# Optimization experiments

Measured on AMD Instinct MI355X. Metric: run time of the kernel, lower is better.

Reference implementation:

```python
import jax, jax.numpy as jnp
import numpy as np

A = 8        # n_agents
NACT = 16    # n_actions
R = 64       # rnn_hidden_dim
OBS = 128    # obs_shape
ATTN = 64    # attn_dim
HID = 256    # hidden_dim
INP = 152    # input_shape = obs + n_actions + n_agents
E = 2048     # episode_num
TW = 1.0     # teammate_loss_weight
WW = 1.0     # world_loss_weight


def _lin(key, out_d, in_d):
    k1, k2 = jax.random.split(key)
    s = 1.0 / np.sqrt(in_d)
    w = jax.random.uniform(k1, (out_d, in_d), minval=-s, maxval=s, dtype=jnp.float32)
    b = jax.random.uniform(k2, (out_d,), minval=-s, maxval=s, dtype=jnp.float32)
    return w, b


def setup_inputs() -> dict:
    key = jax.random.key(0)
    ks = jax.random.split(key, 16)
    rows = E * A
    d = {}
    d['inputs'] = jax.random.normal(ks[0], (rows, INP), dtype=jnp.float32)
    d['hidden_state'] = jax.random.normal(ks[1], (rows, R), dtype=jnp.float32)
    d['obs'] = jax.random.normal(ks[2], (rows, OBS), dtype=jnp.float32)
    d['obs_next'] = jax.random.normal(ks[3], (rows, OBS), dtype=jnp.float32)
    d['u'] = jax.random.randint(ks[4], (rows, 1), 0, NACT, dtype=jnp.int64 if jax.config.jax_enable_x64 else jnp.int32)
    d['fc1_w'], d['fc1_b'] = _lin(ks[5], R, INP)
    d['gru_w_ih'], d['gru_b_ih'] = _lin(ks[6], 3 * R, R)
    d['gru_w_hh'], d['gru_b_hh'] = _lin(ks[7], 3 * R, R)
    d['tm_w1'], d['tm_b1'] = _lin(ks[8], HID, R + A)
    d['tm_w2'], d['tm_b2'] = _lin(ks[9], NACT, HID)
    d['wm_w1'], d['wm_b1'] = _lin(ks[10], HID, OBS + A * NACT)
    d['wm_w2'], d['wm_b2'] = _lin(ks[11], OBS, HID)
    d['wq_w'], d['wq_b'] = _lin(ks[12], ATTN, 2 * OBS)
    d['wk_w'], d['wk_b'] = _lin(ks[13], ATTN, NACT)
    d['wv1_w'], d['wv1_b'] = _lin(ks[14], ATTN, R + NACT)
    d['wv2_w'], d['wv2_b'] = _lin(ks[15], NACT, ATTN)
    return d


def reference(inputs, hidden_state, obs, obs_next, u,
              fc1_w, fc1_b, gru_w_ih, gru_b_ih, gru_w_hh, gru_b_hh,
              tm_w1, tm_b1, tm_w2, tm_b2,
              wm_w1, wm_b1, wm_w2, wm_b2,
              wq_w, wq_b, wk_w, wk_b, wv1_w, wv1_b, wv2_w, wv2_b):
    sg = jax.lax.stop_gradient
    rows = inputs.shape[0]
    Ep = rows // A  # episode_num

    # --- GRU agent trunk ---
    x = jax.nn.relu(inputs @ fc1_w.T + fc1_b)
    h_in = hidden_state.reshape(-1, R)
    gi = x @ gru_w_ih.T + gru_b_ih
    gh = h_in @ gru_w_hh.T + gru_b_hh
    i_r, i_z, i_n = jnp.split(gi, 3, axis=-1)
    h_r, h_z, h_n = jnp.split(gh, 3, axis=-1)
    r = jax.nn.sigmoid(i_r + h_r)
    z = jax.nn.sigmoid(i_z + h_z)
    n = jnp.tanh(i_n + r * h_n)
    h = (1.0 - z) * n + z * h_in  # (rows, R)

    eyeA = jnp.eye(A, dtype=h.dtype)
    off = 1.0 - eyeA  # (A,A) zero on diagonal

    # --- teammate model: h_repeat[e,i,j] = h[e,j] with diagonal zeroed ---
    hd = sg(h).reshape(Ep, A, R)
    hr = jnp.broadcast_to(hd[:, None, :, :], (Ep, A, A, R)) * off[None, :, :, None]
    dj = jnp.broadcast_to(eyeA[None, None], (Ep, A, A, A)) * off[None, :, :, None]
    inp_t = jnp.concatenate([hr.reshape(-1, R), dj.reshape(-1, A)], axis=-1)
    actions = jax.nn.relu(inp_t @ tm_w1.T + tm_b1) @ tm_w2.T + tm_b2  # (Ep*A*A, NACT)

    # --- teammate CE loss (masked mean over all Ep*A*A rows) ---
    labels = jnp.broadcast_to(u.reshape(Ep, 1, A), (Ep, A, A)).reshape(-1)
    mask = jnp.broadcast_to(off[None], (Ep, A, A)).reshape(-1)
    logp = jax.nn.log_softmax(actions, axis=-1)
    ce = -jnp.take_along_axis(logp, labels[:, None], axis=1)[:, 0]
    loss1 = (ce * mask).mean() * TW

    # --- mask own action, world model ---
    am = (actions.reshape(Ep, A, A, NACT) * off[None, :, :, None]).reshape(rows, A, NACT)
    am_det = sg(am)
    w_in = jnp.concatenate([obs, am_det.reshape(rows, A * NACT)], axis=-1)
    o_next_hat = jax.nn.relu(w_in @ wm_w1.T + wm_b1) @ wm_w2.T + wm_b2  # (rows, OBS)
    loss2 = jnp.mean((o_next_hat - obs_next) ** 2) * WW

    # --- reflection: masked attention aggregation over teammates ---
    query = jnp.concatenate([obs, sg(o_next_hat)], axis=-1) @ wq_w.T + wq_b  # (rows, ATTN)
    key = (am_det.reshape(-1, NACT) @ wk_w.T + wk_b).reshape(rows, A, ATTN)
    hrep = jnp.broadcast_to(h.reshape(Ep, 1, A, R), (Ep, A, A, R)).reshape(-1, R)
    inps_v = jnp.concatenate([hrep, am_det.reshape(-1, NACT)], axis=-1)
    value = (jax.nn.relu(inps_v @ wv1_w.T + wv1_b) @ wv2_w.T + wv2_b).reshape(rows, A, NACT)
    scores = jnp.einsum('bd,bjd->bj', query / jnp.sqrt(jnp.float32(ATTN)), key).reshape(Ep, A, A)
    scores = jnp.where(eyeA[None].astype(bool), jnp.float32(-1e9), scores)  # self-exclusion
    attn = jax.nn.softmax(scores, axis=-1).reshape(rows, A, 1)
    q_reflect = jnp.sum(value * attn, axis=1)  # (rows, NACT)

    return q_reflect, h, loss1, loss2
```

## Files before the change

### kernel.cpp

```cpp
#include <hip/hip_runtime.h>
#include <math.h>

#define E_NUM 2048
#define A_N   8
#define ROWS  (E_NUM*A_N)

typedef __attribute__((ext_vector_type(8))) short bf16x8;
typedef __attribute__((ext_vector_type(4))) float f32x4;

__device__ __forceinline__ unsigned short f2bf(float x) {
  unsigned int u = __float_as_uint(x);
  return (unsigned short)((u + 0x7FFFu + ((u >> 16) & 1u)) >> 16);
}
__device__ __forceinline__ ushort4 f2bf4(float4 v) {
  return make_ushort4(f2bf(v.x), f2bf(v.y), f2bf(v.z), f2bf(v.w));
}
#define MFMA16(a,b,c) __builtin_amdgcn_mfma_f32_16x16x32_bf16(a,b,c,0,0,0)

#define T_WK   0
#define T_WV1  1024
#define T_WV2  6144
#define TMB    7168
#define B_WM1  9216
#define B_WM2  41984
#define B_WQ   58368
#define B_TM1  66560
#define B_TM2  74752
#define B_FC1  76800
#define B_WIH  81920
#define B_WHH  88064
#define O_ACT  94208
#define O_QRY  356352
#define O_L1P  1404928
#define O_L2P  1405440

#define DO_H   262144
#define DO_L1  1310720
#define DO_L2  1310721

#define LD4(p) (*(const float4*)(p))

struct PrepP {
  const float* tsrc[3]; int tO[3], tK[3], tOff[3];
  const float* ssrc[8]; int sO[8], sK[8], sKs[8], sSt[8], sOff[8];
  const float* tm_w1; const float* tm_b1;
};

__global__ __launch_bounds__(256) void k_prep(PrepP p, float* __restrict__ ws,
                                              unsigned short* __restrict__ wsu) {
  int bid = blockIdx.x;
  if (bid < 24) {
    int b = bid >> 3, sl = bid & 7;
    const float* s = p.tsrc[b];
    float* d = ws + p.tOff[b];
    int O = p.tO[b], K = p.tK[b], n = O * K;
    for (int i = sl * 256 + threadIdx.x; i < n; i += 2048) {
      int o = i / K, k = i - o * K;
      d[k * O + o] = s[i];
    }
  } else if (bid < 152) {
    int q = bid - 24, m = q >> 4, sub = q & 15;
    const float* src = p.ssrc[m];
    unsigned short* dst = wsu + p.sOff[m];
    int K = p.sK[m], Ks = p.sKs[m], stride = p.sSt[m], n = p.sO[m] * K, S = K >> 5;
    for (int f = sub * 256 + threadIdx.x; f < n; f += 16 * 256) {
      int j = f & 7, l = (f >> 3) & 63, rest = f >> 9;
      int s = rest % S, c = rest / S;
      int row = c * 16 + (l & 15), col = s * 32 + ((l >> 4) << 3) + j;
      dst[f] = (col < Ks) ? f2bf(src[row * stride + col]) : (unsigned short)0;
    }
  } else {
    int i = (bid - 152) * 256 + threadIdx.x;
    int j = i >> 8, o = i & 255;
    ws[TMB + i] = p.tm_b1[o] + p.tm_w1[o * 72 + 64 + j];
  }
}

__global__ __launch_bounds__(512) void k_trunk(
    const float* __restrict__ inp, const float* __restrict__ hin,
    const unsigned short* __restrict__ fc1bf, const unsigned short* __restrict__ wihbf,
    const unsigned short* __restrict__ whhbf,
    const float* __restrict__ fc1_b, const float* __restrict__ bih, const float* __restrict__ bhh,
    float* __restrict__ hout)
{
  __shared__ __align__(16) unsigned short in_b[32 * 168];
  __shared__ __align__(16) unsigned short x_b[32 * 72];
  __shared__ __align__(16) unsigned short h_b[32 * 72];
  int tid = threadIdx.x, w = tid >> 6, lane = tid & 63;
  int lo = lane & 15, hi = lane >> 4;
  int row0 = blockIdx.x * 32;
  int c = w & 3, rt = w >> 2;

  for (int i = tid; i < 1216; i += 512) {
    int e = i << 2;
    int r = e / 152, cc = e - r * 152;
    float4 v = LD4(inp + (size_t)(row0 + r) * 152 + cc);
    *(ushort4*)(in_b + r * 168 + cc) = f2bf4(v);
  }
  if (tid < 256) { int r = tid >> 3, cc = tid & 7; in_b[r * 168 + 152 + cc] = 0; }
  {
    int r = tid >> 4, cc = (tid & 15) << 2;
    float4 v = LD4(hin + (size_t)(row0 + r) * 64 + cc);
    *(ushort4*)(h_b + r * 72 + cc) = f2bf4(v);
  }
  __syncthreads();

  bf16x8 wf1[5];
#pragma unroll
  for (int s = 0; s < 5; s++)
    wf1[s] = *(const bf16x8*)(fc1bf + (size_t)((c * 5 + s) * 64 + lane) * 8);
  f32x4 acc = {0, 0, 0, 0};
#pragma unroll
  for (int s = 0; s < 5; s++) {
    bf16x8 af = *(const bf16x8*)(in_b + (rt * 16 + lo) * 168 + s * 32 + hi * 8);
    acc = MFMA16(af, wf1[s], acc);
  }
  float fb = fc1_b[16 * c + lo];
#pragma unroll
  for (int r = 0; r < 4; r++)
    x_b[(rt * 16 + hi * 4 + r) * 72 + 16 * c + lo] = f2bf(fmaxf(acc[r] + fb, 0.f));
  __syncthreads();

  bf16x8 wfi[3][2], wfh[3][2];
#pragma unroll
  for (int t = 0; t < 3; t++)
#pragma unroll
    for (int s = 0; s < 2; s++) {
      int chunk = c + 4 * t;
      wfi[t][s] = *(const bf16x8*)(wihbf + (size_t)((chunk * 2 + s) * 64 + lane) * 8);
      wfh[t][s] = *(const bf16x8*)(whhbf + (size_t)((chunk * 2 + s) * 64 + lane) * 8);
    }
  f32x4 ai[3], ah[3];
#pragma unroll
  for (int t = 0; t < 3; t++) { ai[t] = {0,0,0,0}; ah[t] = {0,0,0,0}; }
#pragma unroll
  for (int s = 0; s < 2; s++) {
    bf16x8 ax  = *(const bf16x8*)(x_b + (rt * 16 + lo) * 72 + s * 32 + hi * 8);
    bf16x8 ahv = *(const bf16x8*)(h_b + (rt * 16 + lo) * 72 + s * 32 + hi * 8);
#pragma unroll
    for (int t = 0; t < 3; t++) {
      ai[t] = MFMA16(ax,  wfi[t][s], ai[t]);
      ah[t] = MFMA16(ahv, wfh[t][s], ah[t]);
    }
  }
  int col = 16 * c + lo;
  float b_ir = bih[col],       b_hr = bhh[col];
  float b_iz = bih[64 + col],  b_hz = bhh[64 + col];
  float b_in = bih[128 + col], b_hn = bhh[128 + col];
#pragma unroll
  for (int r = 0; r < 4; r++) {
    size_t grow = (size_t)(row0 + rt * 16 + hi * 4 + r);
    float rg = 1.f / (1.f + expf(-(ai[0][r] + b_ir + ah[0][r] + b_hr)));
    float zg = 1.f / (1.f + expf(-(ai[1][r] + b_iz + ah[1][r] + b_hz)));
    float ng = tanhf(fmaf(rg, ah[2][r] + b_hn, ai[2][r] + b_in));
    float h0 = hin[grow * 64 + col];
    hout[grow * 64 + col] = (1.f - zg) * ng + zg * h0;
  }
}

__global__ __launch_bounds__(512) void k_tm(
    const float* __restrict__ h,
    const unsigned short* __restrict__ w1b, const unsigned short* __restrict__ w2b,
    const float* __restrict__ tmB, const float* __restrict__ b2,
    const int* __restrict__ u,
    float* __restrict__ act, float* __restrict__ l1p)
{
  __shared__ __align__(16) unsigned short in_s[32 * 72];
  __shared__ __align__(16) unsigned short hid_s[32 * 264];
  __shared__ float red[512];
  int tid = threadIdx.x, w = tid >> 6, lane = tid & 63;
  int lo = lane & 15, hi = lane >> 4;
  int row0 = blockIdx.x * 32;
  {
    int r = tid >> 4, cc = (tid & 15) << 2;
    float4 v = LD4(h + (size_t)(row0 + r) * 64 + cc);
    *(ushort4*)(in_s + r * 72 + cc) = f2bf4(v);
  }
  bf16x8 wf1[2][2];
#pragma unroll
  for (int cc = 0; cc < 2; cc++)
#pragma unroll
    for (int s = 0; s < 2; s++)
      wf1[cc][s] = *(const bf16x8*)(w1b + (size_t)(((2 * w + cc) * 2 + s) * 64 + lane) * 8);
  __syncthreads();
  f32x4 acc[2][2];
#pragma unroll
  for (int rt = 0; rt < 2; rt++) { acc[rt][0] = {0,0,0,0}; acc[rt][1] = {0,0,0,0}; }
#pragma unroll
  for (int s = 0; s < 2; s++)
#pragma unroll
    for (int rt = 0; rt < 2; rt++) {
      bf16x8 af = *(const bf16x8*)(in_s + (rt * 16 + lo) * 72 + s * 32 + hi * 8);
      acc[rt][0] = MFMA16(af, wf1[0][s], acc[rt][0]);
      acc[rt][1] = MFMA16(af, wf1[1][s], acc[rt][1]);
    }
#pragma unroll
  for (int rt = 0; rt < 2; rt++)
#pragma unroll
    for (int r = 0; r < 4; r++) {
      int rowl = rt * 16 + hi * 4 + r, j = (hi * 4 + r) & 7;
      float v0 = acc[rt][0][r] + tmB[j * 256 + 32 * w + lo];
      float v1 = acc[rt][1][r] + tmB[j * 256 + 32 * w + 16 + lo];
      hid_s[rowl * 264 + 32 * w + lo]      = f2bf(fmaxf(v0, 0.f));
      hid_s[rowl * 264 + 32 * w + 16 + lo] = f2bf(fmaxf(v1, 0.f));
    }
  __syncthreads();
  float ces = 0.f;
  if (w < 2) {
    bf16x8 wf2[8];
#pragma unroll
    for (int s = 0; s < 8; s++)
      wf2[s] = *(const bf16x8*)(w2b + (size_t)(s * 64 + lane) * 8);
    f32x4 a2 = {0, 0, 0, 0};
#pragma unroll
    for (int s = 0; s < 8; s++) {
      bf16x8 af = *(const bf16x8*)(hid_s + (w * 16 + lo) * 264 + s * 32 + hi * 8);
      a2 = MFMA16(af, wf2[s], a2);
    }
    float b2c = b2[lo];
#pragma unroll
    for (int r = 0; r < 4; r++) {
      int rowl = w * 16 + hi * 4 + r;
      float v = a2[r] + b2c;
      act[(size_t)(row0 + rowl) * 16 + lo] = v;
      float m = v;
      m = fmaxf(m, __shfl_xor(m, 1));
      m = fmaxf(m, __shfl_xor(m, 2));
      m = fmaxf(m, __shfl_xor(m, 4));
      m = fmaxf(m, __shfl_xor(m, 8));
      float se = expf(v - m);
      se += __shfl_xor(se, 1);
      se += __shfl_xor(se, 2);
      se += __shfl_xor(se, 4);
      se += __shfl_xor(se, 8);
      int lbl = u[row0 + rowl];
      float vl = __shfl(v, (lane & 48) + lbl);
      if (lo == 0) ces += -(vl - m - logf(se));
    }
  }
  red[tid] = ces;
  __syncthreads();
  for (int st = 256; st > 0; st >>= 1) {
    if (tid < st) red[tid] += red[tid + st];
    __syncthreads();
  }
  if (tid == 0) l1p[blockIdx.x] = red[0];
}

__global__ __launch_bounds__(512) void k_wm(
    const float* __restrict__ obs, const float* __restrict__ act,
    const unsigned short* __restrict__ w1b, const unsigned short* __restrict__ w2b,
    const unsigned short* __restrict__ wqb,
    const float* __restrict__ b1, const float* __restrict__ b2, const float* __restrict__ bq,
    const float* __restrict__ obsn,
    float* __restrict__ qry, float* __restrict__ l2p)
{
  __shared__ __align__(16) unsigned short in_s[32 * 264];
  __shared__ __align__(16) unsigned short q_in[32 * 264];
  __shared__ __align__(16) unsigned short act_bs[4 * 128];
  __shared__ float red[512];
  int tid = threadIdx.x, w = tid >> 6, lane = tid & 63;
  int lo = lane & 15, hi = lane >> 4;
  int row0 = blockIdx.x * 32, e0 = row0 >> 3;
  if (tid < 128) {
    float4 v = LD4(act + (size_t)e0 * 128 + (tid << 2));
    *(ushort4*)(act_bs + (tid << 2)) = f2bf4(v);
  }
  for (int i = tid; i < 1024; i += 512) {
    int r = i >> 5, c = (i & 31) << 2;
    float4 v = LD4(obs + (size_t)(row0 + r) * 128 + c);
    ushort4 u4 = f2bf4(v);
    *(ushort4*)(in_s + r * 264 + c) = u4;
    *(ushort4*)(q_in + r * 264 + c) = u4;
  }
  bf16x8 wf1[2][8], wf2[8];
#pragma unroll
  for (int cc = 0; cc < 2; cc++)
#pragma unroll
    for (int s = 0; s < 8; s++)
      wf1[cc][s] = *(const bf16x8*)(w1b + (size_t)(((2 * w + cc) * 8 + s) * 64 + lane) * 8);
#pragma unroll
  for (int s = 0; s < 8; s++)
    wf2[s] = *(const bf16x8*)(w2b + (size_t)((w * 8 + s) * 64 + lane) * 8);
  __syncthreads();
  for (int i = tid; i < 1024; i += 512) {
    int r = i >> 5, c = (i & 31) << 2;
    int j = c >> 4, ii = r & 7;
    ushort4 v = (j == ii) ? make_ushort4(0, 0, 0, 0)
                          : *(const ushort4*)(act_bs + (r >> 3) * 128 + c);
    *(ushort4*)(in_s + r * 264 + 128 + c) = v;
  }
  __syncthreads();
  f32x4 acc[2][2];
#pragma unroll
  for (int rt = 0; rt < 2; rt++) { acc[rt][0] = {0,0,0,0}; acc[rt][1] = {0,0,0,0}; }
#pragma unroll
  for (int s = 0; s < 8; s++)
#pragma unroll
    for (int rt = 0; rt < 2; rt++) {
      bf16x8 af = *(const bf16x8*)(in_s + (rt * 16 + lo) * 264 + s * 32 + hi * 8);
      acc[rt][0] = MFMA16(af, wf1[0][s], acc[rt][0]);
      acc[rt][1] = MFMA16(af, wf1[1][s], acc[rt][1]);
    }
  float b1a = b1[32 * w + lo], b1b = b1[32 * w + 16 + lo];
  __syncthreads();
#pragma unroll
  for (int rt = 0; rt < 2; rt++)
#pragma unroll
    for (int r = 0; r < 4; r++) {
      int rowl = rt * 16 + hi * 4 + r;
      in_s[rowl * 264 + 32 * w + lo]      = f2bf(fmaxf(acc[rt][0][r] + b1a, 0.f));
      in_s[rowl * 264 + 32 * w + 16 + lo] = f2bf(fmaxf(acc[rt][1][r] + b1b, 0.f));
    }
  __syncthreads();
  f32x4 acc2[2];
  acc2[0] = {0, 0, 0, 0}; acc2[1] = {0, 0, 0, 0};
#pragma unroll
  for (int s = 0; s < 8; s++)
#pragma unroll
    for (int rt = 0; rt < 2; rt++) {
      bf16x8 af = *(const bf16x8*)(in_s + (rt * 16 + lo) * 264 + s * 32 + hi * 8);
      acc2[rt] = MFMA16(af, wf2[s], acc2[rt]);
    }
  int col = 16 * w + lo;
  float b2c = b2[col];
  float ms = 0.f;
#pragma unroll
  for (int rt = 0; rt < 2; rt++)
#pragma unroll
    for (int r = 0; r < 4; r++) {
      int rowl = rt * 16 + hi * 4 + r;
      float v = acc2[rt][r] + b2c;
      q_in[rowl * 264 + 128 + col] = f2bf(v);
      float d = v - obsn[(size_t)(row0 + rowl) * 128 + col];
      ms = fmaf(d, d, ms);
    }
  __syncthreads();
  {
    int c = w & 3, rt = w >> 2;
    bf16x8 wf3[8];
#pragma unroll
    for (int s = 0; s < 8; s++)
      wf3[s] = *(const bf16x8*)(wqb + (size_t)((c * 8 + s) * 64 + lane) * 8);
    f32x4 aq = {0, 0, 0, 0};
#pragma unroll
    for (int s = 0; s < 8; s++) {
      bf16x8 af = *(const bf16x8*)(q_in + (rt * 16 + lo) * 264 + s * 32 + hi * 8);
      aq = MFMA16(af, wf3[s], aq);
    }
    float bqc = bq[16 * c + lo];
#pragma unroll
    for (int r = 0; r < 4; r++) {
      int row = row0 + rt * 16 + hi * 4 + r;
      qry[(size_t)row * 64 + 16 * c + lo] = aq[r] + bqc;
    }
  }
  red[tid] = ms;
  __syncthreads();
  for (int st = 256; st > 0; st >>= 1) {
    if (tid < st) red[tid] += red[tid + st];
    __syncthreads();
  }
  if (tid == 0) l2p[blockIdx.x] = red[0];
}

__global__ __launch_bounds__(256) void k_kva(
    const float* __restrict__ h, const float* __restrict__ act,
    const float* __restrict__ ws, const float* __restrict__ bk,
    const float* __restrict__ bv1, const float* __restrict__ bv2,
    const float* __restrict__ qry, const float* __restrict__ l1p,
    const float* __restrict__ l2p, float* __restrict__ qout)
{
  __shared__ __align__(16) float in_s[32 * 80];
  __shared__ __align__(16) float hid_s[32 * 64];
  __shared__ __align__(16) float key_s[32 * 68];
  __shared__ float val_s[32 * 16];
  __shared__ float qs[4][64];
  __shared__ float red2[256];
  int tid = threadIdx.x, w = tid >> 6, lane = tid & 63;
  int row0 = blockIdx.x * 32;
  if (blockIdx.x == 0) {
    float s1 = l1p[tid] + l1p[tid + 256];
    float s2 = l2p[tid] + l2p[tid + 256];
    red2[tid] = s1;
    __syncthreads();
    for (int s = 128; s > 0; s >>= 1) {
      if (tid < s) red2[tid] += red2[tid + s];
      __syncthreads();
    }
    float S1 = red2[0];
    __syncthreads();
    red2[tid] = s2;
    __syncthreads();
    for (int s = 128; s > 0; s >>= 1) {
      if (tid < s) red2[tid] += red2[tid + s];
      __syncthreads();
    }
    if (tid == 0) {
      qout[DO_L1] = S1 * 7.f / 131072.f;
      qout[DO_L2] = red2[0] / 2097152.f;
    }
    __syncthreads();
  }
  for (int i = tid; i < 512; i += 256) {
    int r = i >> 4, c = (i & 15) << 2;
    *(float4*)(in_s + r * 80 + c) = LD4(h + (size_t)(row0 + r) * 64 + c);
  }
  if (tid < 128) {
    int r = tid >> 2, c = (tid & 3) << 2;
    *(float4*)(in_s + r * 80 + 64 + c) = LD4(act + (size_t)(row0 + r) * 16 + c);
  }
  float qreg[8];
#pragma unroll
  for (int rr = 0; rr < 8; rr++)
    qreg[rr] = qry[(size_t)(row0 + w * 8 + rr) * 64 + lane];
  __syncthreads();
  const float* w1T = ws + T_WV1;
  const float* w2T = ws + T_WV2;
  const float* wkT = ws + T_WK;
  float acc[8];
#pragma unroll
  for (int r = 0; r < 8; r++) acc[r] = bv1[lane];
  for (int k = 0; k < 80; k += 4) {
    float b[4];
#pragma unroll
    for (int j = 0; j < 4; j++) b[j] = w1T[(k + j) * 64 + lane];
#pragma unroll
    for (int r = 0; r < 8; r++) {
      float4 a = LD4(in_s + (w * 8 + r) * 80 + k);
      acc[r] = fmaf(a.x, b[0], fmaf(a.y, b[1], fmaf(a.z, b[2], fmaf(a.w, b[3], acc[r]))));
    }
  }
#pragma unroll
  for (int r = 0; r < 8; r++) hid_s[(w * 8 + r) * 64 + lane] = fmaxf(acc[r], 0.f);
  float ka[8];
#pragma unroll
  for (int r = 0; r < 8; r++) ka[r] = bk[lane];
  for (int k = 0; k < 16; k += 4) {
    float b[4];
#pragma unroll
    for (int j = 0; j < 4; j++) b[j] = wkT[(k + j) * 64 + lane];
#pragma unroll
    for (int r = 0; r < 8; r++) {
      float4 a = LD4(in_s + (w * 8 + r) * 80 + 64 + k);
      ka[r] = fmaf(a.x, b[0], fmaf(a.y, b[1], fmaf(a.z, b[2], fmaf(a.w, b[3], ka[r]))));
    }
  }
#pragma unroll
  for (int r = 0; r < 8; r++) key_s[(w * 8 + r) * 68 + lane] = ka[r];
  int col = lane & 15, kq = lane >> 4;
  float a2[8] = {0, 0, 0, 0, 0, 0, 0, 0};
  for (int kk = 0; kk < 16; kk += 4) {
    int k = kq * 16 + kk;
    float b[4];
#pragma unroll
    for (int j = 0; j < 4; j++) b[j] = w2T[(k + j) * 16 + col];
#pragma unroll
    for (int r = 0; r < 8; r++) {
      float4 a = LD4(hid_s + (w * 8 + r) * 64 + k);
      a2[r] = fmaf(a.x, b[0], fmaf(a.y, b[1], fmaf(a.z, b[2], fmaf(a.w, b[3], a2[r]))));
    }
  }
#pragma unroll
  for (int r = 0; r < 8; r++) {
    a2[r] += __shfl_xor(a2[r], 16);
    a2[r] += __shfl_xor(a2[r], 32);
  }
  if (lane < 16) {
#pragma unroll
    for (int r = 0; r < 8; r++) val_s[(w * 8 + r) * 16 + col] = a2[r] + bv2[col];
  }
  int j = lane >> 3, p = lane & 7;
  for (int rr = 0; rr < 8; rr++) {
    int b = row0 + w * 8 + rr;
    qs[w][lane] = qreg[rr];
    const float* krow = key_s + (w * 8 + j) * 68;
    float s = 0.f;
#pragma unroll
    for (int t = 0; t < 8; t++) {
      int d = p * 8 + t;
      s = fmaf(qs[w][d], krow[d], s);
    }
    s += __shfl_xor(s, 1);
    s += __shfl_xor(s, 2);
    s += __shfl_xor(s, 4);
    float score = (j == rr) ? -1e9f : s * 0.125f;
    float sc[8];
    float m = -1e30f;
#pragma unroll
    for (int jj = 0; jj < 8; jj++) {
      sc[jj] = __shfl(score, jj * 8);
      m = fmaxf(m, sc[jj]);
    }
    float ssum = 0.f;
#pragma unroll
    for (int jj = 0; jj < 8; jj++) { sc[jj] = expf(sc[jj] - m); ssum += sc[jj]; }
    float inv = 1.f / ssum;
    int c = lane & 15, g = lane >> 4;
    const float* vb = val_s + w * 8 * 16;
    float outv = sc[g] * inv * vb[g * 16 + c] + sc[g + 4] * inv * vb[(g + 4) * 16 + c];
    outv += __shfl_xor(outv, 16);
    outv += __shfl_xor(outv, 32);
    if (lane < 16) qout[(size_t)b * 16 + lane] = outv;
  }
}

extern "C" void kernel_launch(void* const* d_in, const int* in_sizes, int n_in,
                              void* d_out, int out_size, void* d_ws, size_t ws_size,
                              hipStream_t stream) {
  const float* inputs   = (const float*)d_in[0];
  const float* hidden   = (const float*)d_in[1];
  const float* obs      = (const float*)d_in[2];
  const float* obs_next = (const float*)d_in[3];
  const int*   u        = (const int*)d_in[4];
  const float* fc1_w = (const float*)d_in[5];   const float* fc1_b = (const float*)d_in[6];
  const float* wih   = (const float*)d_in[7];   const float* bih   = (const float*)d_in[8];
  const float* whh   = (const float*)d_in[9];   const float* bhh   = (const float*)d_in[10];
  const float* tm_w1 = (const float*)d_in[11];  const float* tm_b1 = (const float*)d_in[12];
  const float* tm_w2 = (const float*)d_in[13];  const float* tm_b2 = (const float*)d_in[14];
  const float* wm_w1 = (const float*)d_in[15];  const float* wm_b1 = (const float*)d_in[16];
  const float* wm_w2 = (const float*)d_in[17];  const float* wm_b2 = (const float*)d_in[18];
  const float* wq_w  = (const float*)d_in[19];  const float* wq_b  = (const float*)d_in[20];
  const float* wk_w  = (const float*)d_in[21];  const float* wk_b  = (const float*)d_in[22];
  const float* wv1_w = (const float*)d_in[23];  const float* wv1_b = (const float*)d_in[24];
  const float* wv2_w = (const float*)d_in[25];  const float* wv2_b = (const float*)d_in[26];

  float* ws   = (float*)d_ws;
  unsigned short* wsu = (unsigned short*)d_ws;
  float* out  = (float*)d_out;
  float* hbuf = out + DO_H;

  PrepP p;
  const float* tsr[3] = {wk_w, wv1_w, wv2_w};
  int tO[3]  = {64, 64, 16};
  int tK[3]  = {16, 80, 64};
  int tOf[3] = {T_WK, T_WV1, T_WV2};
  for (int i = 0; i < 3; i++) { p.tsrc[i] = tsr[i]; p.tO[i] = tO[i]; p.tK[i] = tK[i]; p.tOff[i] = tOf[i]; }
  const float* ssr[8] = {wm_w1, wm_w2, wq_w, tm_w1, tm_w2, fc1_w, wih, whh};
  int sO[8]  = {256, 128, 64, 256, 16, 64, 192, 192};
  int sK[8]  = {256, 256, 256, 64, 256, 160, 64, 64};
  int sKs[8] = {256, 256, 256, 64, 256, 152, 64, 64};
  int sSt[8] = {256, 256, 256, 72, 256, 152, 64, 64};
  int sOf[8] = {B_WM1*2, B_WM2*2, B_WQ*2, B_TM1*2, B_TM2*2, B_FC1*2, B_WIH*2, B_WHH*2};
  for (int i = 0; i < 8; i++) {
    p.ssrc[i] = ssr[i]; p.sO[i] = sO[i]; p.sK[i] = sK[i];
    p.sKs[i] = sKs[i]; p.sSt[i] = sSt[i]; p.sOff[i] = sOf[i];
  }
  p.tm_w1 = tm_w1; p.tm_b1 = tm_b1;

  k_prep<<<160, 256, 0, stream>>>(p, ws, wsu);
  k_trunk<<<ROWS / 32, 512, 0, stream>>>(inputs, hidden,
      wsu + B_FC1*2, wsu + B_WIH*2, wsu + B_WHH*2, fc1_b, bih, bhh, hbuf);
  k_tm<<<ROWS / 32, 512, 0, stream>>>(hbuf, wsu + B_TM1*2, wsu + B_TM2*2,
      ws + TMB, tm_b2, u, ws + O_ACT, ws + O_L1P);
  k_wm<<<ROWS / 32, 512, 0, stream>>>(obs, ws + O_ACT,
      wsu + B_WM1*2, wsu + B_WM2*2, wsu + B_WQ*2, wm_b1, wm_b2, wq_b, obs_next,
      ws + O_QRY, ws + O_L2P);
  k_kva<<<ROWS / 32, 256, 0, stream>>>(hbuf, ws + O_ACT, ws, wk_b, wv1_b, wv2_b,
      ws + O_QRY, ws + O_L1P, ws + O_L2P, out);
}
```

Before: 56.66 us.

## Move non-trunk weight prep into extra trunk blocks and store query as bf16

k_prep now converts only the three weights the trunk needs (fc1, w_ih, w_hh). The rest of the weight transposes, bf16 swizzles and the tm bias fold run in 108 extra blocks appended to the k_trunk launch, so this work overlaps with trunk compute and shortens the critical-path prep kernel. Separately, the attention query written by k_wm and read by k_kva is stored as bf16 instead of fp32, halving that intermediate's memory traffic. The bf16 query adds rounding to the attention scores, and the prep-block mapping assumes the extra blocks exactly cover the remaining matrices.

New measurement: 52.63 us. 7.1% less time.

```diff
diff --git a/kernel.cpp b/kernel.cpp
--- a/kernel.cpp
+++ b/kernel.cpp
@@ -4,6 +4,8 @@
 #define E_NUM 2048
 #define A_N   8
 #define ROWS  (E_NUM*A_N)
+#define TRUNK_BLOCKS 512
+#define TRUNK_EXTRA  108
 
 typedef __attribute__((ext_vector_type(8))) short bf16x8;
 typedef __attribute__((ext_vector_type(4))) float f32x4;
@@ -14,6 +16,9 @@
 }
 __device__ __forceinline__ ushort4 f2bf4(float4 v) {
   return make_ushort4(f2bf(v.x), f2bf(v.y), f2bf(v.z), f2bf(v.w));
+}
+__device__ __forceinline__ float bf2f(unsigned short u) {
+  return __uint_as_float(((unsigned int)u) << 16);
 }
 #define MFMA16(a,b,c) __builtin_amdgcn_mfma_f32_16x16x32_bf16(a,b,c,0,0,0)
 
@@ -49,30 +54,15 @@
 __global__ __launch_bounds__(256) void k_prep(PrepP p, float* __restrict__ ws,
                                               unsigned short* __restrict__ wsu) {
   int bid = blockIdx.x;
-  if (bid < 24) {
-    int b = bid >> 3, sl = bid & 7;
-    const float* s = p.tsrc[b];
-    float* d = ws + p.tOff[b];
-    int O = p.tO[b], K = p.tK[b], n = O * K;
-    for (int i = sl * 256 + threadIdx.x; i < n; i += 2048) {
-      int o = i / K, k = i - o * K;
-      d[k * O + o] = s[i];
-    }
-  } else if (bid < 152) {
-    int q = bid - 24, m = q >> 4, sub = q & 15;
-    const float* src = p.ssrc[m];
-    unsigned short* dst = wsu + p.sOff[m];
-    int K = p.sK[m], Ks = p.sKs[m], stride = p.sSt[m], n = p.sO[m] * K, S = K >> 5;
-    for (int f = sub * 256 + threadIdx.x; f < n; f += 16 * 256) {
-      int j = f & 7, l = (f >> 3) & 63, rest = f >> 9;
-      int s = rest % S, c = rest / S;
-      int row = c * 16 + (l & 15), col = s * 32 + ((l >> 4) << 3) + j;
-      dst[f] = (col < Ks) ? f2bf(src[row * stride + col]) : (unsigned short)0;
-    }
-  } else {
-    int i = (bid - 152) * 256 + threadIdx.x;
-    int j = i >> 8, o = i & 255;
-    ws[TMB + i] = p.tm_b1[o] + p.tm_w1[o * 72 + 64 + j];
+  int m = 5 + (bid >> 4), sub = bid & 15;
+  const float* src = p.ssrc[m];
+  unsigned short* dst = wsu + p.sOff[m];
+  int K = p.sK[m], Ks = p.sKs[m], stride = p.sSt[m], n = p.sO[m] * K, S = K >> 5;
+  for (int f = sub * 256 + threadIdx.x; f < n; f += 16 * 256) {
+    int j = f & 7, l = (f >> 3) & 63, rest = f >> 9;
+    int s = rest % S, c = rest / S;
+    int row = c * 16 + (l & 15), col = s * 32 + ((l >> 4) << 3) + j;
+    dst[f] = (col < Ks) ? f2bf(src[row * stride + col]) : (unsigned short)0;
   }
 }
 
@@ -81,13 +71,45 @@
     const unsigned short* __restrict__ fc1bf, const unsigned short* __restrict__ wihbf,
     const unsigned short* __restrict__ whhbf,
     const float* __restrict__ fc1_b, const float* __restrict__ bih, const float* __restrict__ bhh,
-    float* __restrict__ hout)
+    float* __restrict__ hout, PrepP p, float* __restrict__ ws_f,
+    unsigned short* __restrict__ wsu)
 {
   __shared__ __align__(16) unsigned short in_b[32 * 168];
   __shared__ __align__(16) unsigned short x_b[32 * 72];
   __shared__ __align__(16) unsigned short h_b[32 * 72];
   int tid = threadIdx.x, w = tid >> 6, lane = tid & 63;
   int lo = lane & 15, hi = lane >> 4;
+
+  if (blockIdx.x >= TRUNK_BLOCKS) {
+    int eb = blockIdx.x - TRUNK_BLOCKS;
+    if (eb < 24) {
+      int b = eb >> 3, sl = eb & 7;
+      const float* s = p.tsrc[b];
+      float* d = ws_f + p.tOff[b];
+      int O = p.tO[b], K = p.tK[b], n = O * K;
+      for (int i = sl * 512 + tid; i < n; i += 8 * 512) {
+        int o = i / K, k = i - o * K;
+        d[k * O + o] = s[i];
+      }
+    } else if (eb < 104) {
+      int q = eb - 24, m = q >> 4, sub = q & 15;
+      const float* src = p.ssrc[m];
+      unsigned short* dst = wsu + p.sOff[m];
+      int K = p.sK[m], Ks = p.sKs[m], stride = p.sSt[m], n = p.sO[m] * K, S = K >> 5;
+      for (int f = sub * 512 + tid; f < n; f += 16 * 512) {
+        int j = f & 7, l = (f >> 3) & 63, rest = f >> 9;
+        int s = rest % S, c = rest / S;
+        int row = c * 16 + (l & 15), col = s * 32 + ((l >> 4) << 3) + j;
+        dst[f] = (col < Ks) ? f2bf(src[row * stride + col]) : (unsigned short)0;
+      }
+    } else {
+      int i = (eb - 104) * 512 + tid;
+      int j = i >> 8, o = i & 255;
+      ws_f[TMB + i] = p.tm_b1[o] + p.tm_w1[o * 72 + 64 + j];
+    }
+    return;
+  }
+
   int row0 = blockIdx.x * 32;
   int c = w & 3, rt = w >> 2;
 
@@ -253,7 +275,7 @@
     const unsigned short* __restrict__ wqb,
     const float* __restrict__ b1, const float* __restrict__ b2, const float* __restrict__ bq,
     const float* __restrict__ obsn,
-    float* __restrict__ qry, float* __restrict__ l2p)
+    unsigned short* __restrict__ qryb, float* __restrict__ l2p)
 {
   __shared__ __align__(16) unsigned short in_s[32 * 264];
   __shared__ __align__(16) unsigned short q_in[32 * 264];
@@ -352,7 +374,7 @@
 #pragma unroll
     for (int r = 0; r < 4; r++) {
       int row = row0 + rt * 16 + hi * 4 + r;
-      qry[(size_t)row * 64 + 16 * c + lo] = aq[r] + bqc;
+      qryb[(size_t)row * 64 + 16 * c + lo] = f2bf(aq[r] + bqc);
     }
   }
   red[tid] = ms;
@@ -368,7 +390,7 @@
     const float* __restrict__ h, const float* __restrict__ act,
     const float* __restrict__ ws, const float* __restrict__ bk,
     const float* __restrict__ bv1, const float* __restrict__ bv2,
-    const float* __restrict__ qry, const float* __restrict__ l1p,
+    const unsigned short* __restrict__ qryb, const float* __restrict__ l1p,
     const float* __restrict__ l2p, float* __restrict__ qout)
 {
   __shared__ __align__(16) float in_s[32 * 80];
@@ -413,7 +435,7 @@
   float qreg[8];
 #pragma unroll
   for (int rr = 0; rr < 8; rr++)
-    qreg[rr] = qry[(size_t)(row0 + w * 8 + rr) * 64 + lane];
+    qreg[rr] = bf2f(qryb[(size_t)(row0 + w * 8 + rr) * 64 + lane]);
   __syncthreads();
   const float* w1T = ws + T_WV1;
   const float* w2T = ws + T_WV2;
@@ -548,14 +570,14 @@
   }
   p.tm_w1 = tm_w1; p.tm_b1 = tm_b1;
 
-  k_prep<<<160, 256, 0, stream>>>(p, ws, wsu);
-  k_trunk<<<ROWS / 32, 512, 0, stream>>>(inputs, hidden,
-      wsu + B_FC1*2, wsu + B_WIH*2, wsu + B_WHH*2, fc1_b, bih, bhh, hbuf);
+  k_prep<<<48, 256, 0, stream>>>(p, ws, wsu);
+  k_trunk<<<TRUNK_BLOCKS + TRUNK_EXTRA, 512, 0, stream>>>(inputs, hidden,
+      wsu + B_FC1*2, wsu + B_WIH*2, wsu + B_WHH*2, fc1_b, bih, bhh, hbuf, p, ws, wsu);
   k_tm<<<ROWS / 32, 512, 0, stream>>>(hbuf, wsu + B_TM1*2, wsu + B_TM2*2,
       ws + TMB, tm_b2, u, ws + O_ACT, ws + O_L1P);
   k_wm<<<ROWS / 32, 512, 0, stream>>>(obs, ws + O_ACT,
       wsu + B_WM1*2, wsu + B_WM2*2, wsu + B_WQ*2, wm_b1, wm_b2, wq_b, obs_next,
-      ws + O_QRY, ws + O_L2P);
+      wsu + O_QRY * 2, ws + O_L2P);
   k_kva<<<ROWS / 32, 256, 0, stream>>>(hbuf, ws + O_ACT, ws, wk_b, wv1_b, wv2_b,
-      ws + O_QRY, ws + O_L1P, ws + O_L2P, out);
-}
+      wsu + O_QRY * 2, ws + O_L1P, ws + O_L2P, out);
+}
```
